# Performance work log

Hardware: AMD Instinct MI355X
Metric: run time of the kernel (lower is better)

The kernel has to match this reference:

```python
import jax, jax.numpy as jnp
import numpy as np

N = 50000   # nodes
E = 800000  # edges (avg in-degree 16)
H = 4       # attention heads
F = 64      # in/out feats per head
NEG_SLOPE = 0.2  # DGL GATConv default


def setup_inputs() -> dict:
    key = jax.random.key(0)
    ks = jax.random.split(key, 12)
    s = 0.1
    x = jax.random.normal(ks[0], (N, F), jnp.float32)
    src = jax.random.randint(ks[1], (E,), 0, N, jnp.int32)
    dst = jax.random.randint(ks[2], (E,), 0, N, jnp.int32)
    W1 = (jax.random.normal(ks[3], (F, H * F), jnp.float32) * s)
    al1 = (jax.random.normal(ks[4], (H, F), jnp.float32) * s)
    ar1 = (jax.random.normal(ks[5], (H, F), jnp.float32) * s)
    b1 = jnp.zeros((H, F), jnp.float32)
    W2 = (jax.random.normal(ks[6], (F, H * F), jnp.float32) * s)
    al2 = (jax.random.normal(ks[7], (H, F), jnp.float32) * s)
    ar2 = (jax.random.normal(ks[8], (H, F), jnp.float32) * s)
    b2 = jnp.zeros((H, F), jnp.float32)
    return dict(x=x, src=src, dst=dst, W1=W1, al1=al1, ar1=ar1, b1=b1,
                W2=W2, al2=al2, ar2=ar2, b2=b2)


def _gat_layer(x, src, dst, W, al, ar, b):
    # Linear projection, split into heads: [N, H, F]
    h = (x @ W).reshape(N, H, F)
    # Per-node attention logits: [N, H]
    el = jnp.einsum('nhf,hf->nh', h, al)
    er = jnp.einsum('nhf,hf->nh', h, ar)
    # Per-edge score, LeakyReLU: [E, H]
    e = jax.nn.leaky_relu(el[src] + er[dst], NEG_SLOPE)
    # Edge-softmax over incoming edges of each dst node (segment softmax)
    emax = jax.ops.segment_max(e, dst, num_segments=N)        # [N, H]
    ee = jnp.exp(e - emax[dst])                               # [E, H]
    denom = jax.ops.segment_sum(ee, dst, num_segments=N)      # [N, H]
    alpha = ee / denom[dst]                                   # [E, H]
    # Weighted aggregation: gather src feats, scale, scatter-add to dst
    m = h[src] * alpha[..., None]                              # [E, H, F]
    out = jax.ops.segment_sum(m, dst, num_segments=N)          # [N, H, F]
    return out + b[None]


def reference(x, src, dst, W1, al1, ar1, b1, W2, al2, ar2, b2):
    # Layer 1: GATConv with tanh activation, then head-mean
    h = _gat_layer(x, src, dst, W1, al1, ar1, b1)
    h = jnp.tanh(h).mean(axis=-2)              # [N, F]
    # Layer 2: GATConv (no activation), then head-mean
    h = _gat_layer(h, src, dst, W2, al2, ar2, b2)
    return h.mean(axis=-2)                     # [N, F]
```

## Files before the change

kernel.cpp:

```cpp
#include <hip/hip_runtime.h>
#include <hip/hip_fp16.h>
#include <cfloat>
#include <cstddef>

#define NODES 50000
#define EDGES 800000
#define HEADS 4
#define FEAT  64
#define HF    256
#define NEG_SLOPE 0.2f

#define ROWS 32
#define PROJ_BLOCKS ((NODES + ROWS - 1) / ROWS)
#define COUNT_BLOCKS ((EDGES + 255) / 256)


__global__ void zero_deg_kernel(int* __restrict__ deg) {
  int i = blockIdx.x * blockDim.x + threadIdx.x;
  if (i < NODES) deg[i] = 0;
}

#define SCHUNK 13312
#define SPER   13
__global__ __launch_bounds__(1024) void scan_kernel(const int* __restrict__ deg,
                                                    int* __restrict__ rowstart,
                                                    int* __restrict__ cursor) {
  __shared__ int buf[SCHUNK];
  __shared__ int wsum[16];
  __shared__ int carry_s;
  const int tid = threadIdx.x, lane = tid & 63, wv = tid >> 6;
  if (tid == 0) carry_s = 0;
  for (int base = 0; base < NODES; base += SCHUNK) {
    const int sz = min(SCHUNK, NODES - base);
    for (int i = tid; i < sz; i += 1024) buf[i] = deg[base + i];
    __syncthreads();
    const int o = tid * SPER;
    int tsum = 0;
#pragma unroll
    for (int j = 0; j < SPER; ++j) {
      int idx = o + j;
      if (idx < sz) tsum += buf[idx];
    }
    int x = tsum;
#pragma unroll
    for (int off = 1; off < 64; off <<= 1) {
      int u = __shfl_up(x, off, 64);
      if (lane >= off) x += u;
    }
    if (lane == 63) wsum[wv] = x;
    __syncthreads();
    if (wv == 0) {
      int wval = (lane < 16) ? wsum[lane] : 0;
      int wx = wval;
#pragma unroll
      for (int off = 1; off < 16; off <<= 1) {
        int u = __shfl_up(wx, off, 64);
        if (lane >= off) wx += u;
      }
      if (lane < 16) wsum[lane] = wx - wval;
    }
    __syncthreads();
    const int carry = carry_s;
    int run = carry + wsum[wv] + (x - tsum);
#pragma unroll
    for (int j = 0; j < SPER; ++j) {
      int idx = o + j;
      if (idx < sz) { int t = buf[idx]; buf[idx] = run; run += t; }
    }
    __syncthreads();
    for (int i = tid; i < sz; i += 1024) {
      int v = buf[i];
      rowstart[base + i] = v;
      cursor[base + i] = v;
    }
    __syncthreads();
    if (tid == 1023) carry_s = run;
    __syncthreads();
  }
}

__global__ void scatter_kernel(const int* __restrict__ src, const int* __restrict__ dst,
                               int* __restrict__ cursor, int* __restrict__ csr_src) {
  int e = blockIdx.x * blockDim.x + threadIdx.x;
  if (e < EDGES) {
    int pos = atomicAdd(&cursor[dst[e]], 1);
    csr_src[pos] = src[e];
  }
}

__device__ __forceinline__ void proj_body(
    const float* __restrict__ x, const float* __restrict__ W,
    const float* __restrict__ al, const float* __restrict__ ar,
    __half* __restrict__ h, float* __restrict__ el, float* __restrict__ er,
    int blk) {
  __shared__ float xs[ROWS * FEAT];
  const int c = threadIdx.x;
  const int head = c >> 6, f = c & 63;

  float Wc[FEAT];
#pragma unroll
  for (int k = 0; k < FEAT; ++k) Wc[k] = W[k * HF + c];
  const float alv = al[head * FEAT + f];
  const float arv = ar[head * FEAT + f];

  const int row0 = blk * ROWS;
  for (int i = c; i < ROWS * FEAT; i += 256) {
    int r = row0 + (i >> 6);
    xs[i] = (r < NODES) ? x[r * FEAT + (i & 63)] : 0.f;
  }
  __syncthreads();

  for (int r = 0; r < ROWS; ++r) {
    const int row = row0 + r;
    if (row >= NODES) break;
    const float4* xr = (const float4*)&xs[r * FEAT];
    float vs0 = 0.f, vs1 = 0.f, vs2 = 0.f, vs3 = 0.f;
#pragma unroll
    for (int k4 = 0; k4 < 16; k4 += 4) {
      float4 a = xr[k4 + 0];
      float4 b = xr[k4 + 1];
      float4 cc = xr[k4 + 2];
      float4 d = xr[k4 + 3];
      vs0 += a.x * Wc[4 * k4 + 0] + a.y * Wc[4 * k4 + 1] +
             a.z * Wc[4 * k4 + 2] + a.w * Wc[4 * k4 + 3];
      vs1 += b.x * Wc[4 * k4 + 4] + b.y * Wc[4 * k4 + 5] +
             b.z * Wc[4 * k4 + 6] + b.w * Wc[4 * k4 + 7];
      vs2 += cc.x * Wc[4 * k4 + 8] + cc.y * Wc[4 * k4 + 9] +
             cc.z * Wc[4 * k4 + 10] + cc.w * Wc[4 * k4 + 11];
      vs3 += d.x * Wc[4 * k4 + 12] + d.y * Wc[4 * k4 + 13] +
             d.z * Wc[4 * k4 + 14] + d.w * Wc[4 * k4 + 15];
    }
    const float v = (vs0 + vs1) + (vs2 + vs3);
    h[(size_t)row * HF + c] = __float2half(v);
    float sl = v * alv, sr = v * arv;
#pragma unroll
    for (int m = 32; m; m >>= 1) {
      sl += __shfl_xor(sl, m, 64);
      sr += __shfl_xor(sr, m, 64);
    }
    if (f == 0) {
      el[row * HEADS + head] = sl;
      er[row * HEADS + head] = sr;
    }
  }
}

template<int WITH_COUNT>
__global__ __launch_bounds__(256, 2) void proj_kernel(
    const float* __restrict__ x, const float* __restrict__ W,
    const float* __restrict__ al, const float* __restrict__ ar,
    __half* __restrict__ h, float* __restrict__ el, float* __restrict__ er,
    const int* __restrict__ dst, int* __restrict__ deg) {
  if (WITH_COUNT && blockIdx.x >= PROJ_BLOCKS) {
    int e = (blockIdx.x - PROJ_BLOCKS) * 256 + threadIdx.x;
    if (e < EDGES) atomicAdd(&deg[dst[e]], 1);
    return;
  }
  proj_body(x, W, al, ar, h, el, er, blockIdx.x);
}

__device__ __forceinline__ float lrelu(float s) { return s > 0.f ? s : NEG_SLOPE * s; }

__device__ __forceinline__ void gather_fma(const __half* __restrict__ h, int s,
                                           int hh, int fq, float av, float4& acc) {
  union { uint2 u; __half2 h2[2]; } cvt;
  cvt.u = *(const uint2*)(h + (size_t)s * HF + hh * FEAT + fq * 4);
  float2 f01 = __half22float2(cvt.h2[0]);
  float2 f23 = __half22float2(cvt.h2[1]);
  acc.x += f01.x * av;
  acc.y += f01.y * av;
  acc.z += f23.x * av;
  acc.w += f23.y * av;
}

template<int DO_TANH>
__global__ __launch_bounds__(256) void node_kernel(
    const int* __restrict__ rowstart, const int* __restrict__ deg,
    const int* __restrict__ csr_src,
    const float* __restrict__ el, const float* __restrict__ er,
    const __half* __restrict__ h, const float* __restrict__ bias,
    float* __restrict__ out) {
  const int node = (blockIdx.x * blockDim.x + threadIdx.x) >> 6;
  if (node >= NODES) return;
  const int lane = threadIdx.x & 63;
  const int hh = lane >> 4, fq = lane & 15;
  const int rs = rowstart[node];
  const int dg = deg[node];

  float4 acc = make_float4(0.f, 0.f, 0.f, 0.f);

  if (dg > 0) {
    const float4 erv = *(const float4*)&er[node * 4];
    if (dg <= 64) {
      int sL = 0;
      float s0 = -FLT_MAX, s1 = -FLT_MAX, s2 = -FLT_MAX, s3 = -FLT_MAX;
      if (lane < dg) {
        sL = csr_src[rs + lane];
        float4 ev = *(const float4*)&el[sL * 4];
        s0 = lrelu(ev.x + erv.x);
        s1 = lrelu(ev.y + erv.y);
        s2 = lrelu(ev.z + erv.z);
        s3 = lrelu(ev.w + erv.w);
      }
      float m0 = s0, m1 = s1, m2 = s2, m3 = s3;
#pragma unroll
      for (int off = 32; off; off >>= 1) {
        m0 = fmaxf(m0, __shfl_xor(m0, off, 64));
        m1 = fmaxf(m1, __shfl_xor(m1, off, 64));
        m2 = fmaxf(m2, __shfl_xor(m2, off, 64));
        m3 = fmaxf(m3, __shfl_xor(m3, off, 64));
      }
      float E0 = 0.f, E1 = 0.f, E2 = 0.f, E3 = 0.f;
      if (lane < dg) {
        E0 = __expf(s0 - m0);
        E1 = __expf(s1 - m1);
        E2 = __expf(s2 - m2);
        E3 = __expf(s3 - m3);
      }
      float q0 = E0, q1 = E1, q2 = E2, q3 = E3;
#pragma unroll
      for (int off = 32; off; off >>= 1) {
        q0 += __shfl_xor(q0, off, 64);
        q1 += __shfl_xor(q1, off, 64);
        q2 += __shfl_xor(q2, off, 64);
        q3 += __shfl_xor(q3, off, 64);
      }
      const float A0 = E0 / q0, A1 = E1 / q1, A2 = E2 / q2, A3 = E3 / q3;
      for (int i = 0; i < dg; ++i) {
        const int s = __shfl(sL, i, 64);
        const float a0 = __shfl(A0, i, 64);
        const float a1 = __shfl(A1, i, 64);
        const float a2 = __shfl(A2, i, 64);
        const float a3 = __shfl(A3, i, 64);
        const float av = (hh == 0) ? a0 : (hh == 1) ? a1 : (hh == 2) ? a2 : a3;
        gather_fma(h, s, hh, fq, av, acc);
      }
    } else {
      float m0 = -FLT_MAX, m1 = -FLT_MAX, m2 = -FLT_MAX, m3 = -FLT_MAX;
      for (int i = lane; i < dg; i += 64) {
        int s = csr_src[rs + i];
        float4 ev = *(const float4*)&el[s * 4];
        m0 = fmaxf(m0, lrelu(ev.x + erv.x));
        m1 = fmaxf(m1, lrelu(ev.y + erv.y));
        m2 = fmaxf(m2, lrelu(ev.z + erv.z));
        m3 = fmaxf(m3, lrelu(ev.w + erv.w));
      }
#pragma unroll
      for (int off = 32; off; off >>= 1) {
        m0 = fmaxf(m0, __shfl_xor(m0, off, 64));
        m1 = fmaxf(m1, __shfl_xor(m1, off, 64));
        m2 = fmaxf(m2, __shfl_xor(m2, off, 64));
        m3 = fmaxf(m3, __shfl_xor(m3, off, 64));
      }
      float q0 = 0.f, q1 = 0.f, q2 = 0.f, q3 = 0.f;
      for (int i = lane; i < dg; i += 64) {
        int s = csr_src[rs + i];
        float4 ev = *(const float4*)&el[s * 4];
        q0 += __expf(lrelu(ev.x + erv.x) - m0);
        q1 += __expf(lrelu(ev.y + erv.y) - m1);
        q2 += __expf(lrelu(ev.z + erv.z) - m2);
        q3 += __expf(lrelu(ev.w + erv.w) - m3);
      }
#pragma unroll
      for (int off = 32; off; off >>= 1) {
        q0 += __shfl_xor(q0, off, 64);
        q1 += __shfl_xor(q1, off, 64);
        q2 += __shfl_xor(q2, off, 64);
        q3 += __shfl_xor(q3, off, 64);
      }
      const float r0 = 1.f / q0, r1 = 1.f / q1, r2 = 1.f / q2, r3 = 1.f / q3;
      for (int base = 0; base < dg; base += 64) {
        const int cnt = min(64, dg - base);
        int sL = 0;
        float A0 = 0.f, A1 = 0.f, A2 = 0.f, A3 = 0.f;
        if (base + lane < dg) {
          sL = csr_src[rs + base + lane];
          float4 ev = *(const float4*)&el[sL * 4];
          A0 = __expf(lrelu(ev.x + erv.x) - m0) * r0;
          A1 = __expf(lrelu(ev.y + erv.y) - m1) * r1;
          A2 = __expf(lrelu(ev.z + erv.z) - m2) * r2;
          A3 = __expf(lrelu(ev.w + erv.w) - m3) * r3;
        }
        for (int i = 0; i < cnt; ++i) {
          const int s = __shfl(sL, i, 64);
          const float a0 = __shfl(A0, i, 64);
          const float a1 = __shfl(A1, i, 64);
          const float a2 = __shfl(A2, i, 64);
          const float a3 = __shfl(A3, i, 64);
          const float av = (hh == 0) ? a0 : (hh == 1) ? a1 : (hh == 2) ? a2 : a3;
          gather_fma(h, s, hh, fq, av, acc);
        }
      }
    }
  }

  const float4 bv = *(const float4*)&bias[hh * FEAT + fq * 4];
  float vx = acc.x + bv.x, vy = acc.y + bv.y, vz = acc.z + bv.z, vw = acc.w + bv.w;
  if (DO_TANH) { vx = tanhf(vx); vy = tanhf(vy); vz = tanhf(vz); vw = tanhf(vw); }
#pragma unroll
  for (int off = 16; off <= 32; off <<= 1) {
    vx += __shfl_xor(vx, off, 64);
    vy += __shfl_xor(vy, off, 64);
    vz += __shfl_xor(vz, off, 64);
    vw += __shfl_xor(vw, off, 64);
  }
  if (hh == 0) {
    *(float4*)&out[(size_t)node * FEAT + fq * 4] =
        make_float4(vx * 0.25f, vy * 0.25f, vz * 0.25f, vw * 0.25f);
  }
}


extern "C" void kernel_launch(void* const* d_in, const int* in_sizes, int n_in,
                              void* d_out, int out_size, void* d_ws, size_t ws_size,
                              hipStream_t stream) {
  const float* x   = (const float*)d_in[0];
  const int*   src = (const int*)d_in[1];
  const int*   dst = (const int*)d_in[2];
  const float* Ws[2]  = {(const float*)d_in[3], (const float*)d_in[7]};
  const float* als[2] = {(const float*)d_in[4], (const float*)d_in[8]};
  const float* ars[2] = {(const float*)d_in[5], (const float*)d_in[9]};
  const float* bs[2]  = {(const float*)d_in[6], (const float*)d_in[10]};

  float* ws = (float*)d_ws;
  const size_t NHF = (size_t)NODES * HF;
  const size_t NF  = (size_t)NODES * FEAT;
  const size_t NH  = (size_t)NODES * HEADS;
  __half* hbuf = (__half*)ws;
  float* x2   = ws + NHF / 2;
  float* el   = x2 + NF;
  float* er   = el + NH;
  int* ibase   = (int*)(er + NH);
  int* deg      = ibase;
  int* rowstart = ibase + NODES;
  int* cursor   = ibase + 2 * NODES;
  int* csr_src  = ibase + 3 * NODES;
  float* outp = (float*)d_out;

  const int edge_grid = (EDGES + 255) / 256;
  const int node_grid = (NODES * 64) / 256;
  const int n_grid    = (NODES + 255) / 256;

  zero_deg_kernel<<<n_grid, 256, 0, stream>>>(deg);
  proj_kernel<1><<<PROJ_BLOCKS + COUNT_BLOCKS, 256, 0, stream>>>(
      x, Ws[0], als[0], ars[0], hbuf, el, er, dst, deg);
  scan_kernel<<<1, 1024, 0, stream>>>(deg, rowstart, cursor);
  scatter_kernel<<<edge_grid, 256, 0, stream>>>(src, dst, cursor, csr_src);

  node_kernel<1><<<node_grid, 256, 0, stream>>>(rowstart, deg, csr_src, el, er,
                                                hbuf, bs[0], x2);
  proj_kernel<0><<<PROJ_BLOCKS, 256, 0, stream>>>(
      x2, Ws[1], als[1], ars[1], hbuf, el, er, dst, deg);
  node_kernel<0><<<node_grid, 256, 0, stream>>>(rowstart, deg, csr_src, el, er,
                                                hbuf, bs[1], outp);
}
```

Measured before the change: 460.8 us.

## Split projection K dimension across two half-waves with 512-thread blocks

The projection kernel now uses 512 threads per block. Each output column is computed by two lanes, each covering half of the 64-long K dimension, and the halves are combined with a cross-half-wave shuffle. This halves the per-thread W register array (64 to 32), which should lower register pressure and raise occupancy. The per-head attention logits are now reduced through shared memory instead of a full 64-lane shuffle, at the cost of an extra barrier, extra shuffles and redundant lanes doing the half-sums. The degree-count blocks are resized to match the new block size.

Result: slower. 507.1 us (+10.1%).

```diff
diff --git a/kernel.cpp b/kernel.cpp
--- a/kernel.cpp
+++ b/kernel.cpp
@@ -12,7 +12,7 @@
 
 #define ROWS 32
 #define PROJ_BLOCKS ((NODES + ROWS - 1) / ROWS)
-#define COUNT_BLOCKS ((EDGES + 255) / 256)
+#define COUNT_BLOCKS ((EDGES + 511) / 512)
 
 
 __global__ void zero_deg_kernel(int* __restrict__ deg) {
@@ -94,65 +94,72 @@
     __half* __restrict__ h, float* __restrict__ el, float* __restrict__ er,
     int blk) {
   __shared__ float xs[ROWS * FEAT];
-  const int c = threadIdx.x;
+  __shared__ float ehp[2][ROWS][8];
+  const int tid = threadIdx.x;
+  const int wv = tid >> 6;
+  const int lane = tid & 63;
+  const int kh = lane >> 5;
+  const int c = wv * 32 + (lane & 31);
   const int head = c >> 6, f = c & 63;
 
-  float Wc[FEAT];
-#pragma unroll
-  for (int k = 0; k < FEAT; ++k) Wc[k] = W[k * HF + c];
+  float Wc[32];
+#pragma unroll
+  for (int k = 0; k < 32; ++k) Wc[k] = W[(kh * 32 + k) * HF + c];
   const float alv = al[head * FEAT + f];
   const float arv = ar[head * FEAT + f];
 
   const int row0 = blk * ROWS;
-  for (int i = c; i < ROWS * FEAT; i += 256) {
+  for (int i = tid; i < ROWS * FEAT; i += 512) {
     int r = row0 + (i >> 6);
-    xs[i] = (r < NODES) ? x[r * FEAT + (i & 63)] : 0.f;
+    xs[i] = (r < NODES) ? x[(size_t)r * FEAT + (i & 63)] : 0.f;
   }
   __syncthreads();
 
   for (int r = 0; r < ROWS; ++r) {
     const int row = row0 + r;
     if (row >= NODES) break;
-    const float4* xr = (const float4*)&xs[r * FEAT];
-    float vs0 = 0.f, vs1 = 0.f, vs2 = 0.f, vs3 = 0.f;
-#pragma unroll
-    for (int k4 = 0; k4 < 16; k4 += 4) {
-      float4 a = xr[k4 + 0];
-      float4 b = xr[k4 + 1];
-      float4 cc = xr[k4 + 2];
-      float4 d = xr[k4 + 3];
-      vs0 += a.x * Wc[4 * k4 + 0] + a.y * Wc[4 * k4 + 1] +
-             a.z * Wc[4 * k4 + 2] + a.w * Wc[4 * k4 + 3];
-      vs1 += b.x * Wc[4 * k4 + 4] + b.y * Wc[4 * k4 + 5] +
-             b.z * Wc[4 * k4 + 6] + b.w * Wc[4 * k4 + 7];
-      vs2 += cc.x * Wc[4 * k4 + 8] + cc.y * Wc[4 * k4 + 9] +
-             cc.z * Wc[4 * k4 + 10] + cc.w * Wc[4 * k4 + 11];
-      vs3 += d.x * Wc[4 * k4 + 12] + d.y * Wc[4 * k4 + 13] +
-             d.z * Wc[4 * k4 + 14] + d.w * Wc[4 * k4 + 15];
-    }
-    const float v = (vs0 + vs1) + (vs2 + vs3);
-    h[(size_t)row * HF + c] = __float2half(v);
+    const float4* xr = (const float4*)&xs[r * FEAT + kh * 32];
+    float va = 0.f, vb = 0.f;
+#pragma unroll
+    for (int q = 0; q < 8; q += 2) {
+      float4 a = xr[q], b = xr[q + 1];
+      va += a.x * Wc[4 * q + 0] + a.y * Wc[4 * q + 1] +
+            a.z * Wc[4 * q + 2] + a.w * Wc[4 * q + 3];
+      vb += b.x * Wc[4 * q + 4] + b.y * Wc[4 * q + 5] +
+            b.z * Wc[4 * q + 6] + b.w * Wc[4 * q + 7];
+    }
+    float v = va + vb;
+    v += __shfl_xor(v, 32, 64);
+    if (kh == 0) h[(size_t)row * HF + c] = __float2half(v);
     float sl = v * alv, sr = v * arv;
 #pragma unroll
-    for (int m = 32; m; m >>= 1) {
+    for (int m = 1; m <= 16; m <<= 1) {
       sl += __shfl_xor(sl, m, 64);
       sr += __shfl_xor(sr, m, 64);
     }
-    if (f == 0) {
-      el[row * HEADS + head] = sl;
-      er[row * HEADS + head] = sr;
+    if (lane == 0) { ehp[0][r][wv] = sl; ehp[1][r][wv] = sr; }
+  }
+  __syncthreads();
+  for (int i = tid; i < 2 * ROWS * HEADS; i += 512) {
+    const int sel = (i >= ROWS * HEADS) ? 1 : 0;
+    const int j = i - sel * ROWS * HEADS;
+    const int r = j >> 2, hd = j & 3;
+    const int row = row0 + r;
+    if (row < NODES) {
+      float s = ehp[sel][r][hd * 2 + 0] + ehp[sel][r][hd * 2 + 1];
+      (sel ? er : el)[row * HEADS + hd] = s;
     }
   }
 }
 
 template<int WITH_COUNT>
-__global__ __launch_bounds__(256, 2) void proj_kernel(
+__global__ __launch_bounds__(512, 2) void proj_kernel(
     const float* __restrict__ x, const float* __restrict__ W,
     const float* __restrict__ al, const float* __restrict__ ar,
     __half* __restrict__ h, float* __restrict__ el, float* __restrict__ er,
     const int* __restrict__ dst, int* __restrict__ deg) {
   if (WITH_COUNT && blockIdx.x >= PROJ_BLOCKS) {
-    int e = (blockIdx.x - PROJ_BLOCKS) * 256 + threadIdx.x;
+    int e = (blockIdx.x - PROJ_BLOCKS) * 512 + threadIdx.x;
     if (e < EDGES) atomicAdd(&deg[dst[e]], 1);
     return;
   }
@@ -342,14 +349,14 @@
   const int n_grid    = (NODES + 255) / 256;
 
   zero_deg_kernel<<<n_grid, 256, 0, stream>>>(deg);
-  proj_kernel<1><<<PROJ_BLOCKS + COUNT_BLOCKS, 256, 0, stream>>>(
+  proj_kernel<1><<<PROJ_BLOCKS + COUNT_BLOCKS, 512, 0, stream>>>(
       x, Ws[0], als[0], ars[0], hbuf, el, er, dst, deg);
   scan_kernel<<<1, 1024, 0, stream>>>(deg, rowstart, cursor);
   scatter_kernel<<<edge_grid, 256, 0, stream>>>(src, dst, cursor, csr_src);
 
   node_kernel<1><<<node_grid, 256, 0, stream>>>(rowstart, deg, csr_src, el, er,
                                                 hbuf, bs[0], x2);
-  proj_kernel<0><<<PROJ_BLOCKS, 256, 0, stream>>>(
+  proj_kernel<0><<<PROJ_BLOCKS, 512, 0, stream>>>(
       x2, Ws[1], als[1], ars[1], hbuf, el, er, dst, deg);
   node_kernel<0><<<node_grid, 256, 0, stream>>>(rowstart, deg, csr_src, el, er,
                                                 hbuf, bs[1], outp);
```
